# Kernel tuning notes

Measured on AMD Instinct MI355X. Metric: run time of the kernel, lower is better.

## Reference

```python
import jax, jax.numpy as jnp
import numpy as np

N_FILES = 256      # number of files (segments)
LINES = 128        # lines per file
T = N_FILES * LINES  # total lines = 32768
D_ENC = 768        # CodeBERT hidden size
HID = 256          # GCN hidden_dim
SD = 128           # shared_dim
PD = 128           # private_dim
WINDOW = 2         # line-graph window
S_AM = 30.0        # AM-Softmax scale
M_AM = 0.35        # AM-Softmax margin


def _build_edges():
    # build_line_graph: connect lines within a file at offsets 1..WINDOW, both directions
    idx = np.arange(T)
    srcs, dsts = [], []
    for off in range(1, WINDOW + 1):
        m = (idx % LINES) + off < LINES  # j stays inside the same file
        i = idx[m]; j = i + off
        srcs += [i, j]; dsts += [j, i]
    return np.stack([np.concatenate(srcs), np.concatenate(dsts)]).astype(np.int32)


def setup_inputs() -> dict:
    key = jax.random.key(0)
    ks = jax.random.split(key, 18)
    std = 0.02
    inp = {
        "line_emb": jax.random.normal(ks[0], (T, D_ENC), jnp.float32),
        "W1": jax.random.normal(ks[1], (D_ENC, HID), jnp.float32) * std,
        "b1": jnp.zeros((HID,), jnp.float32),
        "W2": jax.random.normal(ks[2], (HID, HID), jnp.float32) * std,
        "b2": jnp.zeros((HID,), jnp.float32),
        "attn_w": jax.random.normal(ks[3], (HID, 1), jnp.float32) * std,
        "attn_b": jnp.zeros((1,), jnp.float32),
        "Ws": jax.random.normal(ks[4], (HID, SD), jnp.float32) * std,
        "bs": jnp.zeros((SD,), jnp.float32),
        "Wp": jax.random.normal(ks[5], (HID, PD), jnp.float32) * std,
        "bp": jnp.zeros((PD,), jnp.float32),
        "cls_w": jax.random.normal(ks[6], (SD, 2), jnp.float32) * std,
        "Wd1": jax.random.normal(ks[7], (SD, SD), jnp.float32) * std,
        "bd1": jnp.zeros((SD,), jnp.float32),
        "Wd2": jax.random.normal(ks[8], (SD, 2), jnp.float32) * std,
        "bd2": jnp.zeros((2,), jnp.float32),
        "line_ptr": jnp.arange(0, T + 1, LINES, dtype=jnp.int32),
        "edge_index": jnp.asarray(_build_edges()),
        "file_labels": jax.random.randint(ks[9], (N_FILES,), 0, 2, jnp.int32),
    }
    return inp


def _l2norm(x):
    return x / jnp.maximum(jnp.linalg.norm(x, axis=1, keepdims=True), 1e-12)


def _gcn(x, W, b, src, dst, n):
    sl = jnp.arange(n, dtype=src.dtype)
    src = jnp.concatenate([src, sl]); dst = jnp.concatenate([dst, sl])
    deg = jax.ops.segment_sum(jnp.ones_like(src, jnp.float32), dst, num_segments=n)
    norm = jax.lax.rsqrt(deg[src] * deg[dst])  # [E+n]
    h = x @ W                                   # [n, out]
    msg = h[src] * norm[:, None]
    return jax.ops.segment_sum(msg, dst, num_segments=n) + b


def reference(line_emb, W1, b1, W2, b2, attn_w, attn_b, Ws, bs, Wp, bp,
              cls_w, Wd1, bd1, Wd2, bd2, line_ptr, edge_index, file_labels):
    n = line_emb.shape[0]
    n_files = line_ptr.shape[0] - 1
    src, dst = edge_index[0], edge_index[1]

    h = jax.nn.relu(_gcn(line_emb, W1, b1, src, dst, n))
    h = _gcn(h, W2, b2, src, dst, n)               # [T, HID]

    # ragged per-file softmax attention pooling
    seg = jnp.searchsorted(line_ptr, jnp.arange(n, dtype=line_ptr.dtype), side="right") - 1
    logits = (h @ attn_w).squeeze(-1) + attn_b[0]  # [T]
    seg_max = jax.ops.segment_max(logits, seg, num_segments=n_files)
    e = jnp.exp(logits - seg_max[seg])
    denom = jax.ops.segment_sum(e, seg, num_segments=n_files)
    att_weights = e / denom[seg]
    h_file = jax.ops.segment_sum(att_weights[:, None] * h, seg, num_segments=n_files)  # [N, HID]

    # disentangle heads
    z_shared = h_file @ Ws + bs
    z_private = h_file @ Wp + bp

    # AM-Softmax classifier (labels given -> subtract margin on true class)
    cos = _l2norm(z_shared) @ (cls_w / jnp.maximum(jnp.linalg.norm(cls_w, axis=0, keepdims=True), 1e-12))
    onehot = jax.nn.one_hot(file_labels, 2, dtype=cos.dtype)
    logits_cls = S_AM * (cos - M_AM * onehot)

    # orthogonality loss
    corr = _l2norm(z_shared).T @ _l2norm(z_private)
    ortho = jnp.linalg.norm(corr)

    # domain discriminator (GRL is identity in forward)
    domain_logits = jax.nn.relu(z_shared @ Wd1 + bd1) @ Wd2 + bd2

    return (logits_cls, h_file, z_shared, z_private, att_weights, domain_logits, ortho)
```

## Files before the change

### kernel.cpp

```cpp
#include <hip/hip_runtime.h>


typedef __attribute__((ext_vector_type(8))) short bf16x8;
typedef __attribute__((ext_vector_type(4))) short bf16x4;
typedef __attribute__((ext_vector_type(4))) float f32x4;
typedef __attribute__((ext_vector_type(8))) float f32x8;

__device__ __forceinline__ unsigned short f2bf(float f) {
  union { float f; unsigned int i; } v; v.f = f;
  unsigned int r = v.i + 0x7FFFu + ((v.i >> 16) & 1u);
  return (unsigned short)(r >> 16);
}
__device__ __forceinline__ float bf2f(unsigned short u) {
  union { unsigned int i; float f; } v; v.i = ((unsigned int)u) << 16; return v.f;
}
__device__ __forceinline__ float cvt4dot(bf16x4 v, f32x4* o) {
  (*o)[0] = bf2f(((unsigned short*)&v)[0]); (*o)[1] = bf2f(((unsigned short*)&v)[1]);
  (*o)[2] = bf2f(((unsigned short*)&v)[2]); (*o)[3] = bf2f(((unsigned short*)&v)[3]);
  return 0.f;
}
__device__ __forceinline__ int degf(int p) {
  return 5 - (p < 2 ? 2 - p : 0) - (p > 125 ? p - 125 : 0);
}
__device__ __forceinline__ float wsum(float v) {
#pragma unroll
  for (int o = 1; o < 64; o <<= 1) v += __shfl_xor(v, o);
  return v;
}

__global__ void prep_weights(const float* __restrict__ W1, const float* __restrict__ W2,
                             const float* __restrict__ Ws, const float* __restrict__ Wp,
                             const float* __restrict__ Wd1,
                             unsigned short* __restrict__ W1t, unsigned short* __restrict__ W2t,
                             unsigned short* __restrict__ WsbG, unsigned short* __restrict__ WpbG,
                             unsigned short* __restrict__ Wd1bG) {
  __shared__ float tile[32][33];
  int id = blockIdx.x;
  int tx = threadIdx.x, ty = threadIdx.y;
  if (id >= 256) {
    int id2 = id - 256;
    const float* src; unsigned short* dst; int blk;
    if (id2 < 32)      { src = Ws;  dst = WsbG;  blk = id2; }
    else if (id2 < 64) { src = Wp;  dst = WpbG;  blk = id2 - 32; }
    else               { src = Wd1; dst = Wd1bG; blk = id2 - 64; }
    int tid = ty * 32 + tx;
    int e0 = blk * 1024 + tid * 4;
    f32x4 v = *(const f32x4*)&src[e0];
    unsigned short o[4];
#pragma unroll
    for (int j = 0; j < 4; ++j) o[j] = f2bf(v[j]);
    *(bf16x4*)&dst[e0] = *(bf16x4*)o;
    return;
  }
  const float* src; unsigned short* dst; int R, C, bx, by;
  if (id < 192) { src = W1; dst = W1t; R = 768; C = 256; bx = (id % 8) * 32; by = (id / 8) * 32; }
  else { id -= 192; src = W2; dst = W2t; R = 256; C = 256; bx = (id % 8) * 32; by = (id / 8) * 32; }
#pragma unroll
  for (int j = 0; j < 32; j += 8)
    tile[ty + j][tx] = src[(by + ty + j) * C + bx + tx];
  __syncthreads();
#pragma unroll
  for (int j = 0; j < 32; j += 8)
    dst[(bx + ty + j) * R + by + tx] = f2bf(tile[tx][ty + j]);
}

__global__ __launch_bounds__(1024) void mega(const float* __restrict__ A,
    const unsigned short* __restrict__ W1t, const float* __restrict__ b1,
    const unsigned short* __restrict__ W2t, const float* __restrict__ b2,
    const float* __restrict__ attn_w, const float* __restrict__ attn_b,
    const unsigned short* __restrict__ WsbG, const float* __restrict__ bs,
    const unsigned short* __restrict__ WpbG, const float* __restrict__ bp,
    const float* __restrict__ cls_w, const int* __restrict__ labels,
    const unsigned short* __restrict__ Wd1bG, const float* __restrict__ bd1,
    const float* __restrict__ Wd2, const float* __restrict__ bd2,
    float* __restrict__ zsn_g, float* __restrict__ zpn_g,
    float* __restrict__ out) {
  __shared__ __align__(16) char lds[131072];
  unsigned short* sA1 = (unsigned short*)lds;
  unsigned short* sB1 = (unsigned short*)(lds + 32768);
  unsigned short* H1  = (unsigned short*)lds;
  unsigned short* G1L = (unsigned short*)(lds + 65536);
  unsigned short* sB2 = (unsigned short*)lds;
  unsigned short* H2  = (unsigned short*)lds;
  unsigned short* hB  = (unsigned short*)(lds + 65536);
  unsigned short* Wlo = (unsigned short*)lds;
  unsigned short* Whi = (unsigned short*)(lds + 65536);
  __shared__ float awS[256];
  __shared__ float lgS[128];
  __shared__ float redM[64];
  __shared__ float scr[1024];
  __shared__ float hfS[256];
  __shared__ float zsS[128], zpS[128], znS[128];
  __shared__ float redS[16];

  const int t = threadIdx.x;
  const int wave = t >> 6, lane = t & 63;
  const int wr = wave >> 2, wc = wave & 3;
  const int file = blockIdx.x;
  const long rowA = (long)file * 128;

  if (t < 256) awS[t] = attn_w[t];

  f32x4 acc[2][4];
#pragma unroll
  for (int m = 0; m < 2; ++m)
#pragma unroll
    for (int n = 0; n < 4; ++n) acc[m][n] = (f32x4)0.0f;

  const int arow = t >> 3, acol = (t & 7) * 8;
  const int aswz = arow * 64 + (acol ^ ((arow & 7) << 3));
  f32x8 areg;
#define ISSUE_A1(kt) areg = *(const f32x8*)&A[(rowA + arow) * 768 + (kt) * 64 + acol]
#define WRITE_A1(buf) { unsigned short u[8];                                      \
    _Pragma("unroll") for (int j = 0; j < 8; ++j) u[j] = f2bf(areg[j]);           \
    *(bf16x8*)&sA1[(buf) * 8192 + aswz] = *(bf16x8*)u; }
#define ISSUE_B1(kt, buf) _Pragma("unroll") for (int it = 0; it < 2; ++it) {      \
    int flat = (it * 1024 + t) * 8;                                               \
    int n = flat >> 6, k = flat & 63;                                             \
    const unsigned short* g = W1t + n * 768 + (kt) * 64 + (k ^ ((n & 7) << 3));   \
    __builtin_amdgcn_global_load_lds(                                             \
        (const __attribute__((address_space(1))) unsigned int*)g,                 \
        (__attribute__((address_space(3))) unsigned int*)                         \
            &sB1[(buf) * 16384 + (it * 16 + wave) * 512], 16, 0, 0); }

  ISSUE_A1(0); ISSUE_B1(0, 0); WRITE_A1(0);
  __syncthreads();
  for (int kt = 0; kt < 12; ++kt) {
    const int cur = kt & 1, nxt = cur ^ 1;
    if (kt + 1 < 12) { ISSUE_A1(kt + 1); ISSUE_B1(kt + 1, nxt); }
#pragma unroll
    for (int kk = 0; kk < 2; ++kk) {
      const int kb = kk * 32 + (lane >> 4) * 8;
      bf16x8 af[2], bfr[4];
#pragma unroll
      for (int m = 0; m < 2; ++m) {
        int r = wr * 32 + m * 16 + (lane & 15);
        af[m] = *(const bf16x8*)&sA1[cur * 8192 + r * 64 + (kb ^ ((r & 7) << 3))];
      }
#pragma unroll
      for (int n = 0; n < 4; ++n) {
        int r = wc * 64 + n * 16 + (lane & 15);
        bfr[n] = *(const bf16x8*)&sB1[cur * 16384 + r * 64 + (kb ^ ((r & 7) << 3))];
      }
#pragma unroll
      for (int m = 0; m < 2; ++m)
#pragma unroll
        for (int n = 0; n < 4; ++n)
          acc[m][n] = __builtin_amdgcn_mfma_f32_16x16x32_bf16(af[m], bfr[n], acc[m][n], 0, 0, 0);
    }
    if (kt + 1 < 12) WRITE_A1(nxt);
    __syncthreads();
  }
#pragma unroll
  for (int m = 0; m < 2; ++m)
#pragma unroll
    for (int n = 0; n < 4; ++n) {
      int r = wr * 32 + m * 16 + (lane >> 4) * 4;
      int c = wc * 64 + n * 16 + (lane & 15);
#pragma unroll
      for (int j = 0; j < 4; ++j) H1[(r + j) * 256 + c] = f2bf(acc[m][n][j]);
    }
  __syncthreads();
#pragma unroll
  for (int it = 0; it < 8; ++it) {
    int g = it * 1024 + t;
    int l = g >> 6, c0 = (g & 63) * 4;
    int dl = degf(l);
    f32x4 s = (f32x4)0.0f;
#pragma unroll
    for (int o = -2; o <= 2; ++o) {
      int q = l + o;
      if (q < 0 || q > 127) continue;
      float w = __frsqrt_rn((float)(dl * degf(q)));
      bf16x4 hv4 = *(const bf16x4*)&H1[q * 256 + c0];
      f32x4 hv; cvt4dot(hv4, &hv);
      s += w * hv;
    }
    f32x4 b = *(const f32x4*)&b1[c0];
    unsigned short o4[4];
#pragma unroll
    for (int j = 0; j < 4; ++j) o4[j] = f2bf(fmaxf(s[j] + b[j], 0.f));
    *(bf16x4*)&G1L[l * 256 + (c0 ^ ((l & 7) << 3))] = *(bf16x4*)o4;
  }
  __syncthreads();

#pragma unroll
  for (int m = 0; m < 2; ++m)
#pragma unroll
    for (int n = 0; n < 4; ++n) acc[m][n] = (f32x4)0.0f;
#define ISSUE_B2(kt, buf) _Pragma("unroll") for (int it = 0; it < 2; ++it) {      \
    int flat = (it * 1024 + t) * 8;                                               \
    int n = flat >> 6, k = flat & 63;                                             \
    const unsigned short* g = W2t + n * 256 + (kt) * 64 + (k ^ ((n & 7) << 3));   \
    __builtin_amdgcn_global_load_lds(                                             \
        (const __attribute__((address_space(1))) unsigned int*)g,                 \
        (__attribute__((address_space(3))) unsigned int*)                         \
            &sB2[(buf) * 16384 + (it * 16 + wave) * 512], 16, 0, 0); }

  ISSUE_B2(0, 0);
  __syncthreads();
  for (int kt = 0; kt < 4; ++kt) {
    const int cur = kt & 1, nxt = cur ^ 1;
    if (kt + 1 < 4) ISSUE_B2(kt + 1, nxt);
#pragma unroll
    for (int kk = 0; kk < 2; ++kk) {
      const int kb = kk * 32 + (lane >> 4) * 8;
      bf16x8 af[2], bfr[4];
#pragma unroll
      for (int m = 0; m < 2; ++m) {
        int r = wr * 32 + m * 16 + (lane & 15);
        int col = kt * 64 + kb;
        af[m] = *(const bf16x8*)&G1L[r * 256 + (col ^ ((r & 7) << 3))];
      }
#pragma unroll
      for (int n = 0; n < 4; ++n) {
        int r = wc * 64 + n * 16 + (lane & 15);
        bfr[n] = *(const bf16x8*)&sB2[cur * 16384 + r * 64 + (kb ^ ((r & 7) << 3))];
      }
#pragma unroll
      for (int m = 0; m < 2; ++m)
#pragma unroll
        for (int n = 0; n < 4; ++n)
          acc[m][n] = __builtin_amdgcn_mfma_f32_16x16x32_bf16(af[m], bfr[n], acc[m][n], 0, 0, 0);
    }
    __syncthreads();
  }
#pragma unroll
  for (int m = 0; m < 2; ++m)
#pragma unroll
    for (int n = 0; n < 4; ++n) {
      int r = wr * 32 + m * 16 + (lane >> 4) * 4;
      int c = wc * 64 + n * 16 + (lane & 15);
#pragma unroll
      for (int j = 0; j < 4; ++j) H2[(r + j) * 256 + c] = f2bf(acc[m][n][j]);
    }
  __syncthreads();
#pragma unroll
  for (int it = 0; it < 8; ++it) {
    int g = it * 1024 + t;
    int l = g >> 6, c0 = (g & 63) * 4;
    int dl = degf(l);
    f32x4 s = (f32x4)0.0f;
#pragma unroll
    for (int o = -2; o <= 2; ++o) {
      int q = l + o;
      if (q < 0 || q > 127) continue;
      float w = __frsqrt_rn((float)(dl * degf(q)));
      bf16x4 hv4 = *(const bf16x4*)&H2[q * 256 + c0];
      f32x4 hv; cvt4dot(hv4, &hv);
      s += w * hv;
    }
    f32x4 b = *(const f32x4*)&b2[c0];
    unsigned short o4[4];
#pragma unroll
    for (int j = 0; j < 4; ++j) o4[j] = f2bf(s[j] + b[j]);
    *(bf16x4*)&hB[l * 256 + c0] = *(bf16x4*)o4;
  }
  __syncthreads();
#define ISSUE_WB(srcG, dstL, rounds) _Pragma("unroll") for (int it = 0; it < (rounds); ++it) { \
    const unsigned short* g = (srcG) + (it * 1024 + t) * 8;                        \
    __builtin_amdgcn_global_load_lds(                                              \
        (const __attribute__((address_space(1))) unsigned int*)g,                  \
        (__attribute__((address_space(3))) unsigned int*)                          \
            &(dstL)[(it * 16 + wave) * 512], 16, 0, 0); }
  ISSUE_WB(WsbG, Wlo, 4);

  {
    int l = t >> 3, p = t & 7;
    float part = 0.f;
#pragma unroll 4
    for (int j = 0; j < 32; ++j) {
      int c = p * 32 + ((j + 4 * p + l) & 31);
      part += bf2f(hB[l * 256 + c]) * awS[c];
    }
    part += __shfl_xor(part, 1);
    part += __shfl_xor(part, 2);
    part += __shfl_xor(part, 4);
    if (p == 0) lgS[l] = part + attn_b[0];
  }
  __syncthreads();
  if (t < 64) redM[t] = fmaxf(lgS[t], lgS[t + 64]);
  __syncthreads();
  for (int s = 32; s > 0; s >>= 1) {
    if (t < s) redM[t] = fmaxf(redM[t], redM[t + s]);
    __syncthreads();
  }
  float mx = redM[0];
  __syncthreads();
  if (t < 128) lgS[t] = expf(lgS[t] - mx);
  __syncthreads();
  if (t < 64) redM[t] = lgS[t] + lgS[t + 64];
  __syncthreads();
  for (int s = 32; s > 0; s >>= 1) {
    if (t < s) redM[t] += redM[t + s];
    __syncthreads();
  }
  float dn = redM[0];
  __syncthreads();
  if (t < 128) {
    float w = lgS[t] / dn;
    lgS[t] = w;
    out[131584 + file * 128 + t] = w;
  }
  __syncthreads();
  {
    int c = t & 255, grp = t >> 8;
    float s = 0.f;
    for (int l = grp * 32; l < grp * 32 + 32; ++l) s += lgS[l] * bf2f(hB[l * 256 + c]);
    scr[grp * 256 + c] = s;
  }
  __syncthreads();
  if (t < 256) {
    float tot = scr[t] + scr[256 + t] + scr[512 + t] + scr[768 + t];
    hfS[t] = tot;
    out[512 + file * 256 + t] = tot;
  }
  __syncthreads();

  ISSUE_WB(WpbG, Whi, 4);
  {
    int g = t >> 7, j = t & 127;
    float s = 0.f;
#pragma unroll 8
    for (int c = g * 32; c < g * 32 + 32; ++c) s += hfS[c] * bf2f(Wlo[c * 128 + j]);
    scr[g * 128 + j] = s;
  }
  __syncthreads();
  ISSUE_WB(Wd1bG, Wlo, 2);
  if (t < 128) {
    float zs = bs[t];
#pragma unroll
    for (int g = 0; g < 8; ++g) zs += scr[g * 128 + t];
    zsS[t] = zs;
    out[66048 + file * 128 + t] = zs;
    float s = wsum(zs * zs);
    if (lane == 0) redS[wave] = s;
  }
  __syncthreads();
  if (t == 0) redS[8] = fmaxf(sqrtf(redS[0] + redS[1]), 1e-12f);
  {
    int g = t >> 7, j = t & 127;
    float s = 0.f;
#pragma unroll 8
    for (int c = g * 32; c < g * 32 + 32; ++c) s += hfS[c] * bf2f(Whi[c * 128 + j]);
    scr[g * 128 + j] = s;
  }
  __syncthreads();
  if (t < 128) {
    float zsn = zsS[t] / redS[8];
    znS[t] = zsn;
    zsn_g[file * 128 + t] = zsn;
  } else if (t < 256) {
    int j = t - 128;
    float zp = bp[j];
#pragma unroll
    for (int g = 0; g < 8; ++g) zp += scr[g * 128 + j];
    zpS[j] = zp;
    out[98816 + file * 128 + j] = zp;
    float s = wsum(zp * zp);
    if (lane == 0) redS[10 + (wave - 2)] = s;
  }
  __syncthreads();
  if (t == 0) redS[9] = fmaxf(sqrtf(redS[10] + redS[11]), 1e-12f);
  __syncthreads();
  if (t < 128) zpn_g[file * 128 + t] = zpS[t] / redS[9];
  {
    int j = t & 127;
    if (t < 512) {
      float v;
      if (t < 128)       v = znS[j] * cls_w[j * 2 + 0];
      else if (t < 256)  v = znS[j] * cls_w[j * 2 + 1];
      else if (t < 384)  { float w0 = cls_w[j * 2 + 0]; v = w0 * w0; }
      else               { float w1 = cls_w[j * 2 + 1]; v = w1 * w1; }
      float s = wsum(v);
      if (lane == 0) redS[wave] = s;
    }
  }
  __syncthreads();
  if (t == 0) {
    float d0 = redS[0] + redS[1], d1 = redS[2] + redS[3];
    float n0 = fmaxf(sqrtf(redS[4] + redS[5]), 1e-12f);
    float n1 = fmaxf(sqrtf(redS[6] + redS[7]), 1e-12f);
    int lab = labels[file];
    out[file * 2 + 0] = 30.0f * (d0 / n0 - 0.35f * (lab == 0 ? 1.f : 0.f));
    out[file * 2 + 1] = 30.0f * (d1 / n1 - 0.35f * (lab == 1 ? 1.f : 0.f));
  }
  __syncthreads();
  {
    int g = t >> 7, j = t & 127;
    float s = 0.f;
#pragma unroll 8
    for (int a = g * 16; a < g * 16 + 16; ++a) s += zsS[a] * bf2f(Wlo[a * 128 + j]);
    scr[g * 128 + j] = s;
  }
  __syncthreads();
  if (t < 128) {
    float dd = bd1[t];
#pragma unroll
    for (int g = 0; g < 8; ++g) dd += scr[g * 128 + t];
    dd = fmaxf(dd, 0.f);
    float s0 = wsum(dd * Wd2[t * 2 + 0]);
    if (lane == 0) redS[wave] = s0;
    float s1 = wsum(dd * Wd2[t * 2 + 1]);
    if (lane == 0) redS[4 + wave] = s1;
  }
  __syncthreads();
  if (t == 0) {
    out[164352 + file * 2 + 0] = redS[0] + redS[1] + bd2[0];
    out[164352 + file * 2 + 1] = redS[4] + redS[5] + bd2[1];
  }
#undef ISSUE_A1
#undef WRITE_A1
#undef ISSUE_B1
#undef ISSUE_B2
#undef ISSUE_WB
}

__global__ __launch_bounds__(128) void ortho_partial(const float* __restrict__ zsn,
                                                     const float* __restrict__ zpn,
                                                     float* __restrict__ partial) {
  const int a = blockIdx.x, b = threadIdx.x;
  float s = 0.f;
  for (int f = 0; f < 256; ++f) s += zsn[f * 128 + a] * zpn[f * 128 + b];
  __shared__ float red[128];
  red[b] = s * s; __syncthreads();
  for (int st = 64; st > 0; st >>= 1) { if (b < st) red[b] += red[b + st]; __syncthreads(); }
  if (b == 0) partial[a] = red[0];
}

__global__ __launch_bounds__(128) void ortho_final(const float* __restrict__ partial,
                                                   float* __restrict__ out) {
  const int t = threadIdx.x;
  __shared__ float red[128];
  red[t] = partial[t]; __syncthreads();
  for (int st = 64; st > 0; st >>= 1) { if (t < st) red[t] += red[t + st]; __syncthreads(); }
  if (t == 0) out[164864] = sqrtf(red[0]);
}

extern "C" void kernel_launch(void* const* d_in, const int* in_sizes, int n_in,
                              void* d_out, int out_size, void* d_ws, size_t ws_size,
                              hipStream_t stream) {
  const float* line_emb = (const float*)d_in[0];
  const float* W1     = (const float*)d_in[1];
  const float* b1     = (const float*)d_in[2];
  const float* W2     = (const float*)d_in[3];
  const float* b2     = (const float*)d_in[4];
  const float* attn_w = (const float*)d_in[5];
  const float* attn_b = (const float*)d_in[6];
  const float* Ws     = (const float*)d_in[7];
  const float* bs     = (const float*)d_in[8];
  const float* Wp     = (const float*)d_in[9];
  const float* bp     = (const float*)d_in[10];
  const float* cls_w  = (const float*)d_in[11];
  const float* Wd1    = (const float*)d_in[12];
  const float* bd1    = (const float*)d_in[13];
  const float* Wd2    = (const float*)d_in[14];
  const float* bd2    = (const float*)d_in[15];
  const int* labels   = (const int*)d_in[18];

  char* ws = (char*)d_ws;
  unsigned short* W1t  = (unsigned short*)(ws + 0);
  unsigned short* W2t  = (unsigned short*)(ws + 393216);
  float* zsn           = (float*)(ws + 524288);
  float* zpn           = (float*)(ws + 655360);
  float* partial       = (float*)(ws + 786432);
  unsigned short* WsbG = (unsigned short*)(ws + 1048576);
  unsigned short* WpbG = (unsigned short*)(ws + 1114112);
  unsigned short* Wd1bG= (unsigned short*)(ws + 1179648);
  float* out           = (float*)d_out;

  prep_weights<<<dim3(336), dim3(32, 8), 0, stream>>>(W1, W2, Ws, Wp, Wd1,
                                                      W1t, W2t, WsbG, WpbG, Wd1bG);
  mega<<<dim3(256), dim3(1024), 0, stream>>>(line_emb, W1t, b1, W2t, b2,
                                             attn_w, attn_b, WsbG, bs, WpbG, bp,
                                             cls_w, labels, Wd1bG, bd1, Wd2, bd2,
                                             zsn, zpn, out);
  ortho_partial<<<dim3(128), dim3(128), 0, stream>>>(zsn, zpn, partial);
  ortho_final<<<dim3(1), dim3(128), 0, stream>>>(partial, out);
}
```

Measured before the change: 70.46 us.

## Split first GEMM into separate 512-block kernel writing H1 to global

Moves the 768->256 GEMM out of the fused per-file megakernel into its own kernel with 64-row tiles and 512 blocks, writing bf16 H1 to workspace. The megakernel then loads H1 from global memory into LDS and continues as before. The aim is to double the grid and use more CUs for the dominant GEMM. In exchange it adds a kernel launch and a global round trip of H1, and the A tile is now single-buffered, costing an extra barrier per k-step.

```diff
diff --git a/kernel.cpp b/kernel.cpp
--- a/kernel.cpp
+++ b/kernel.cpp
@@ -64,8 +64,84 @@
     dst[(bx + ty + j) * R + by + tx] = f2bf(tile[tx][ty + j]);
 }
 
-__global__ __launch_bounds__(1024) void mega(const float* __restrict__ A,
-    const unsigned short* __restrict__ W1t, const float* __restrict__ b1,
+__global__ __launch_bounds__(512) void gemm1(const float* __restrict__ A,
+                                             const unsigned short* __restrict__ W1t,
+                                             unsigned short* __restrict__ H1g) {
+  __shared__ __align__(16) char lds[73728];
+  unsigned short* sA = (unsigned short*)lds;
+  unsigned short* sB = (unsigned short*)(lds + 8192);
+  const int t = threadIdx.x;
+  const int wave = t >> 6, lane = t & 63;
+  const int wr = wave >> 2, wc = wave & 3;
+  const long rowA = (long)blockIdx.x * 64;
+
+  f32x4 acc[2][4];
+#pragma unroll
+  for (int m = 0; m < 2; ++m)
+#pragma unroll
+    for (int n = 0; n < 4; ++n) acc[m][n] = (f32x4)0.0f;
+
+  const int arow = t >> 3, acol = (t & 7) * 8;
+  const int aswz = arow * 64 + (acol ^ ((arow & 7) << 3));
+  f32x8 areg;
+#define G1_ISSUE_A(kt) areg = *(const f32x8*)&A[(rowA + arow) * 768 + (kt) * 64 + acol]
+#define G1_WRITE_A() { unsigned short u[8];                                       \
+    _Pragma("unroll") for (int j = 0; j < 8; ++j) u[j] = f2bf(areg[j]);           \
+    *(bf16x8*)&sA[aswz] = *(bf16x8*)u; }
+#define G1_ISSUE_B(kt, buf) _Pragma("unroll") for (int it = 0; it < 4; ++it) {    \
+    int flat = (it * 512 + t) * 8;                                                \
+    int n = flat >> 6, k = flat & 63;                                             \
+    const unsigned short* g = W1t + n * 768 + (kt) * 64 + (k ^ ((n & 7) << 3));   \
+    __builtin_amdgcn_global_load_lds(                                             \
+        (const __attribute__((address_space(1))) unsigned int*)g,                 \
+        (__attribute__((address_space(3))) unsigned int*)                         \
+            &sB[(buf) * 16384 + (it * 8 + wave) * 512], 16, 0, 0); }
+
+  G1_ISSUE_A(0); G1_ISSUE_B(0, 0); G1_WRITE_A();
+  __syncthreads();
+  for (int kt = 0; kt < 12; ++kt) {
+    const int cur = kt & 1, nxt = cur ^ 1;
+    if (kt + 1 < 12) { G1_ISSUE_A(kt + 1); G1_ISSUE_B(kt + 1, nxt); }
+#pragma unroll
+    for (int kk = 0; kk < 2; ++kk) {
+      const int kb = kk * 32 + (lane >> 4) * 8;
+      bf16x8 af[2], bfr[4];
+#pragma unroll
+      for (int m = 0; m < 2; ++m) {
+        int r = wr * 32 + m * 16 + (lane & 15);
+        af[m] = *(const bf16x8*)&sA[r * 64 + (kb ^ ((r & 7) << 3))];
+      }
+#pragma unroll
+      for (int n = 0; n < 4; ++n) {
+        int r = wc * 64 + n * 16 + (lane & 15);
+        bfr[n] = *(const bf16x8*)&sB[cur * 16384 + r * 64 + (kb ^ ((r & 7) << 3))];
+      }
+#pragma unroll
+      for (int m = 0; m < 2; ++m)
+#pragma unroll
+        for (int n = 0; n < 4; ++n)
+          acc[m][n] = __builtin_amdgcn_mfma_f32_16x16x32_bf16(af[m], bfr[n], acc[m][n], 0, 0, 0);
+    }
+    __syncthreads();
+    if (kt + 1 < 12) G1_WRITE_A();
+    __syncthreads();
+  }
+#pragma unroll
+  for (int m = 0; m < 2; ++m)
+#pragma unroll
+    for (int n = 0; n < 4; ++n) {
+      int r = wr * 32 + m * 16 + (lane >> 4) * 4;
+      int c = wc * 64 + n * 16 + (lane & 15);
+#pragma unroll
+      for (int j = 0; j < 4; ++j) H1g[(rowA + r + j) * 256 + c] = f2bf(acc[m][n][j]);
+    }
+#undef G1_ISSUE_A
+#undef G1_WRITE_A
+#undef G1_ISSUE_B
+}
+
+__global__ __launch_bounds__(1024) void mega2(const unsigned short* __restrict__ H1g,
+    const float* __restrict__ b1,
     const unsigned short* __restrict__ W2t, const float* __restrict__ b2,
     const float* __restrict__ attn_w, const float* __restrict__ attn_b,
     const unsigned short* __restrict__ WsbG, const float* __restrict__ bs,
@@ -76,8 +152,6 @@
     float* __restrict__ zsn_g, float* __restrict__ zpn_g,
     float* __restrict__ out) {
   __shared__ __align__(16) char lds[131072];
-  unsigned short* sA1 = (unsigned short*)lds;
-  unsigned short* sB1 = (unsigned short*)(lds + 32768);
   unsigned short* H1  = (unsigned short*)lds;
   unsigned short* G1L = (unsigned short*)(lds + 65536);
   unsigned short* sB2 = (unsigned short*)lds;
@@ -101,65 +175,14 @@
 
   if (t < 256) awS[t] = attn_w[t];
 
-  f32x4 acc[2][4];
-#pragma unroll
-  for (int m = 0; m < 2; ++m)
-#pragma unroll
-    for (int n = 0; n < 4; ++n) acc[m][n] = (f32x4)0.0f;
-
-  const int arow = t >> 3, acol = (t & 7) * 8;
-  const int aswz = arow * 64 + (acol ^ ((arow & 7) << 3));
-  f32x8 areg;
-#define ISSUE_A1(kt) areg = *(const f32x8*)&A[(rowA + arow) * 768 + (kt) * 64 + acol]
-#define WRITE_A1(buf) { unsigned short u[8];                                      \
-    _Pragma("unroll") for (int j = 0; j < 8; ++j) u[j] = f2bf(areg[j]);           \
-    *(bf16x8*)&sA1[(buf) * 8192 + aswz] = *(bf16x8*)u; }
-#define ISSUE_B1(kt, buf) _Pragma("unroll") for (int it = 0; it < 2; ++it) {      \
-    int flat = (it * 1024 + t) * 8;                                               \
-    int n = flat >> 6, k = flat & 63;                                             \
-    const unsigned short* g = W1t + n * 768 + (kt) * 64 + (k ^ ((n & 7) << 3));   \
-    __builtin_amdgcn_global_load_lds(                                             \
-        (const __attribute__((address_space(1))) unsigned int*)g,                 \
-        (__attribute__((address_space(3))) unsigned int*)                         \
-            &sB1[(buf) * 16384 + (it * 16 + wave) * 512], 16, 0, 0); }
-
-  ISSUE_A1(0); ISSUE_B1(0, 0); WRITE_A1(0);
-  __syncthreads();
-  for (int kt = 0; kt < 12; ++kt) {
-    const int cur = kt & 1, nxt = cur ^ 1;
-    if (kt + 1 < 12) { ISSUE_A1(kt + 1); ISSUE_B1(kt + 1, nxt); }
-#pragma unroll
-    for (int kk = 0; kk < 2; ++kk) {
-      const int kb = kk * 32 + (lane >> 4) * 8;
-      bf16x8 af[2], bfr[4];
-#pragma unroll
-      for (int m = 0; m < 2; ++m) {
-        int r = wr * 32 + m * 16 + (lane & 15);
-        af[m] = *(const bf16x8*)&sA1[cur * 8192 + r * 64 + (kb ^ ((r & 7) << 3))];
-      }
-#pragma unroll
-      for (int n = 0; n < 4; ++n) {
-        int r = wc * 64 + n * 16 + (lane & 15);
-        bfr[n] = *(const bf16x8*)&sB1[cur * 16384 + r * 64 + (kb ^ ((r & 7) << 3))];
-      }
-#pragma unroll
-      for (int m = 0; m < 2; ++m)
-#pragma unroll
-        for (int n = 0; n < 4; ++n)
-          acc[m][n] = __builtin_amdgcn_mfma_f32_16x16x32_bf16(af[m], bfr[n], acc[m][n], 0, 0, 0);
-    }
-    if (kt + 1 < 12) WRITE_A1(nxt);
-    __syncthreads();
-  }
-#pragma unroll
-  for (int m = 0; m < 2; ++m)
-#pragma unroll
-    for (int n = 0; n < 4; ++n) {
-      int r = wr * 32 + m * 16 + (lane >> 4) * 4;
-      int c = wc * 64 + n * 16 + (lane & 15);
-#pragma unroll
-      for (int j = 0; j < 4; ++j) H1[(r + j) * 256 + c] = f2bf(acc[m][n][j]);
-    }
+#pragma unroll
+  for (int it = 0; it < 4; ++it) {
+    const unsigned short* g = H1g + rowA * 256 + (it * 1024 + t) * 8;
+    __builtin_amdgcn_global_load_lds(
+        (const __attribute__((address_space(1))) unsigned int*)g,
+        (__attribute__((address_space(3))) unsigned int*)&H1[(it * 16 + wave) * 512],
+        16, 0, 0);
+  }
   __syncthreads();
 #pragma unroll
   for (int it = 0; it < 8; ++it) {
@@ -184,6 +207,7 @@
   }
   __syncthreads();
 
+  f32x4 acc[2][4];
 #pragma unroll
   for (int m = 0; m < 2; ++m)
 #pragma unroll
@@ -409,9 +433,6 @@
     out[164352 + file * 2 + 0] = redS[0] + redS[1] + bd2[0];
     out[164352 + file * 2 + 1] = redS[4] + redS[5] + bd2[1];
   }
-#undef ISSUE_A1
-#undef WRITE_A1
-#undef ISSUE_B1
 #undef ISSUE_B2
 #undef ISSUE_WB
 }
@@ -467,14 +488,16 @@
   unsigned short* WsbG = (unsigned short*)(ws + 1048576);
   unsigned short* WpbG = (unsigned short*)(ws + 1114112);
   unsigned short* Wd1bG= (unsigned short*)(ws + 1179648);
+  unsigned short* H1g  = (unsigned short*)(ws + 2097152);
   float* out           = (float*)d_out;
 
   prep_weights<<<dim3(336), dim3(32, 8), 0, stream>>>(W1, W2, Ws, Wp, Wd1,
                                                       W1t, W2t, WsbG, WpbG, Wd1bG);
-  mega<<<dim3(256), dim3(1024), 0, stream>>>(line_emb, W1t, b1, W2t, b2,
-                                             attn_w, attn_b, WsbG, bs, WpbG, bp,
-                                             cls_w, labels, Wd1bG, bd1, Wd2, bd2,
-                                             zsn, zpn, out);
+  gemm1<<<dim3(512), dim3(512), 0, stream>>>(line_emb, W1t, H1g);
+  mega2<<<dim3(256), dim3(1024), 0, stream>>>(H1g, b1, W2t, b2,
+                                              attn_w, attn_b, WsbG, bs, WpbG, bp,
+                                              cls_w, labels, Wd1bG, bd1, Wd2, bd2,
+                                              zsn, zpn, out);
   ortho_partial<<<dim3(128), dim3(128), 0, stream>>>(zsn, zpn, partial);
   ortho_final<<<dim3(1), dim3(128), 0, stream>>>(partial, out);
 }
```

After: 72.56 us. 1.03x slower.
